# Kernel optimization log

Hardware: AMD Instinct MI355X
Metric: run time of the kernel (lower is better)

The kernel has to match this reference:

```python
import jax, jax.numpy as jnp
import numpy as np

N_NODE = 100_000
N_EDGE = 1_000_000
D = 64          # in_dim = out_dim
A = 64          # attn_dim
B = 8           # batchsize
N_REL = 200     # rel table size = 2*n_rel+1 = 401
N_ENT = 50_000
N_RELTAB = 2 * N_REL + 1


def setup_inputs() -> dict:
    key = jax.random.key(0)
    ks = jax.random.split(key, 16)
    # edges columns: [batch_query_idx, head_ent, rel, tail_ent, sub_local, obj_local]
    r_idx = jax.random.randint(ks[0], (N_EDGE,), 0, B)
    head = jax.random.randint(ks[1], (N_EDGE,), 0, N_ENT)
    rel = jax.random.randint(ks[2], (N_EDGE,), 0, N_RELTAB)
    tail = jax.random.randint(ks[3], (N_EDGE,), 0, N_ENT)
    sub = jax.random.randint(ks[4], (N_EDGE,), 0, N_NODE)
    obj = jax.random.randint(ks[5], (N_EDGE,), 0, N_NODE)
    edges = jnp.stack([r_idx, head, rel, tail, sub, obj], axis=1)
    nodes = jnp.stack([
        jax.random.randint(ks[6], (N_NODE,), 0, B),
        jax.random.randint(ks[7], (N_NODE,), 0, N_ENT)], axis=1)
    s = 1.0 / np.sqrt(D)
    return {
        "q_sub": jax.random.randint(ks[8], (B,), 0, N_ENT),
        "q_rel": jax.random.randint(ks[9], (B,), 0, N_RELTAB),
        "hidden": jax.random.normal(ks[10], (N_NODE, D), jnp.float32),
        "edges": edges,
        "nodes": nodes,
        "old_nodes_new_idx": jax.random.randint(ks[11], (50_000,), 0, N_NODE),
        "batchsize": B,
        "rel_emb": jax.random.normal(ks[12], (N_RELTAB, D), jnp.float32) * s,
        "Ws": jax.random.normal(ks[13], (A, D), jnp.float32) * s,
        "Wr": jax.random.normal(ks[14], (A, D), jnp.float32) * s,
        "Wqr_w": jax.random.normal(ks[15], (A, D), jnp.float32) * s,
        "Wqr_b": jnp.zeros((A,), jnp.float32),
        "walpha_w": jax.random.normal(jax.random.fold_in(key, 101), (1, A), jnp.float32) * (1.0 / np.sqrt(A)),
        "walpha_b": jnp.zeros((1,), jnp.float32),
        "Wh": jax.random.normal(jax.random.fold_in(key, 102), (D, D), jnp.float32) * s,
    }


def reference(q_sub, q_rel, hidden, edges, nodes, old_nodes_new_idx, batchsize,
              rel_emb, Ws, Wr, Wqr_w, Wqr_b, walpha_w, walpha_b, Wh):
    sub = edges[:, 4]   # local source node index [E]
    rel = edges[:, 2]   # relation index        [E]
    obj = edges[:, 5]   # local target node     [E]
    r_idx = edges[:, 0]  # which query each edge belongs to [E]

    hs = hidden[sub]                 # [E, D] gather of node hidden states
    hr = rel_emb[rel]                # [E, D] relation embedding (rela_embed(h, r) = rel_emb[r])
    h_qr = rel_emb[q_rel][r_idx]     # [E, D] query relation embedding per edge

    # attention MLP: sigmoid(w_alpha @ relu(Ws hs + Wr hr + Wqr h_qr + b))
    pre = (jnp.einsum('ed,ad->ea', hs, Ws)
           + jnp.einsum('ed,ad->ea', hr, Wr)
           + jnp.einsum('ed,ad->ea', h_qr, Wqr_w) + Wqr_b)        # [E, A]
    alpha = jax.nn.sigmoid(jnp.einsum('ea,oa->eo', jax.nn.relu(pre), walpha_w) + walpha_b)  # [E, 1]

    message = alpha * (hs + hr)      # [E, D]
    n_node = hidden.shape[0]
    message_agg = jax.ops.segment_sum(message, obj, num_segments=n_node)  # [N, D]
    hidden_new = jnp.einsum('nd,od->no', message_agg, Wh)  # act = identity
    return hidden_new
```

## Files before the change

kernel.cpp:

```cpp
#include <hip/hip_runtime.h>
#include <cstdint>
#include <cstddef>

#define DD 64
#define N_RELTAB 401
#define N_QR 8
#define T_ROWS (N_RELTAB + N_QR)
#define T_U16_STRIDE 66

__device__ __forceinline__ uint16_t f2bf(float f) {
    uint32_t u = __float_as_uint(f);
    u += 0x7fffu + ((u >> 16) & 1u);
    return (uint16_t)(u >> 16);
}
__device__ __forceinline__ float bf2f(uint16_t u) {
    return __uint_as_float(((uint32_t)u) << 16);
}

__global__ __launch_bounds__(64) void build_T(
    const float* __restrict__ rel_emb, const float* __restrict__ Wr,
    const float* __restrict__ Wqr_w, const float* __restrict__ Wqr_b,
    const int* __restrict__ q_rel, uint16_t* __restrict__ T)
{
    int r = blockIdx.x, a = threadIdx.x;
    const float* w;
    const float* src;
    float acc;
    if (r < N_RELTAB) { w = Wr + a * DD; src = rel_emb + r * DD; acc = 0.f; }
    else {
        int k = r - N_RELTAB;
        w = Wqr_w + a * DD;
        src = rel_emb + q_rel[k] * DD;
        acc = Wqr_b[a];
    }
#pragma unroll
    for (int d = 0; d < DD; ++d) acc = fmaf(src[d], w[d], acc);
    T[r * T_U16_STRIDE + a] = f2bf(acc);
}

__global__ __launch_bounds__(256) void rowmat(
    const float* __restrict__ in, const float* __restrict__ W,
    float* __restrict__ out, int nrows)
{
    int n = blockIdx.x * 256 + threadIdx.x;
    if (n >= nrows) return;
    float row[DD];
    const float4* rp = (const float4*)(in + ((size_t)n << 6));
#pragma unroll
    for (int j = 0; j < DD / 4; ++j) {
        float4 v = rp[j];
        row[4*j+0] = v.x; row[4*j+1] = v.y; row[4*j+2] = v.z; row[4*j+3] = v.w;
    }
    float4* op = (float4*)(out + ((size_t)n << 6));
    for (int a0 = 0; a0 < DD; a0 += 4) {
        const float* w0 = W + a0 * DD;
        float s0 = 0.f, s1 = 0.f, s2 = 0.f, s3 = 0.f;
#pragma unroll
        for (int d = 0; d < DD; ++d) {
            float r = row[d];
            s0 = fmaf(w0[d],          r, s0);
            s1 = fmaf(w0[DD + d],     r, s1);
            s2 = fmaf(w0[2 * DD + d], r, s2);
            s3 = fmaf(w0[3 * DD + d], r, s3);
        }
        float4 o; o.x = s0; o.y = s1; o.z = s2; o.w = s3;
        op[a0 >> 2] = o;
    }
}

__global__ __launch_bounds__(256) void hist_kernel(
    const int* __restrict__ edges, int* __restrict__ counts, int n_edge)
{
    int e = blockIdx.x * 256 + threadIdx.x;
    if (e < n_edge) atomicAdd(&counts[edges[6 * e + 5]], 1);
}

__global__ __launch_bounds__(1024) void scan1(
    const int* __restrict__ counts, int* __restrict__ offsets,
    int* __restrict__ bsums, int n)
{
    __shared__ int wsum[16];
    int t = threadIdx.x, i = blockIdx.x * 1024 + t;
    int lane = t & 63, wid = t >> 6;
    int c = (i < n) ? counts[i] : 0;
    int v = c;
#pragma unroll
    for (int d = 1; d < 64; d <<= 1) { int u = __shfl_up(v, d); if (lane >= d) v += u; }
    if (lane == 63) wsum[wid] = v;
    __syncthreads();
    if (wid == 0) {
        int s = (lane < 16) ? wsum[lane] : 0;
#pragma unroll
        for (int d = 1; d < 16; d <<= 1) { int u = __shfl_up(s, d); if (lane >= d) s += u; }
        if (lane < 16) wsum[lane] = s;
    }
    __syncthreads();
    int woff = (wid == 0) ? 0 : wsum[wid - 1];
    if (i < n) offsets[i] = woff + v - c;
    if (t == 1023) bsums[blockIdx.x] = wsum[15];
}

__global__ void scan2(const int* __restrict__ bsums, int* __restrict__ boffs, int nb)
{
    if (threadIdx.x == 0 && blockIdx.x == 0) {
        int s = 0;
        for (int i = 0; i < nb; ++i) { boffs[i] = s; s += bsums[i]; }
    }
}

__global__ __launch_bounds__(1024) void scan3(
    int* __restrict__ offsets, int* __restrict__ cursor,
    const int* __restrict__ boffs, int n)
{
    int i = blockIdx.x * 1024 + threadIdx.x;
    if (i < n) {
        int v = offsets[i] + boffs[blockIdx.x];
        offsets[i] = v;
        cursor[i] = v;
    }
}

__global__ __launch_bounds__(256) void build_sorted(
    const int* __restrict__ edges, int* __restrict__ cursor,
    uint32_t* __restrict__ sorted, int n_edge)
{
    int e = blockIdx.x * 256 + threadIdx.x;
    if (e >= n_edge) return;
    const int2* ep = (const int2*)(edges + 6 * e);
    int ridx = ep[0].x;
    int rel  = ep[1].x;
    int2 so  = ep[2];
    int pos = atomicAdd(&cursor[so.y], 1);
    sorted[pos] = (uint32_t)so.x | ((uint32_t)rel << 17) | ((uint32_t)ridx << 26);
}

__global__ __launch_bounds__(256) void aggregate(
    const uint32_t* __restrict__ sorted, const int* __restrict__ offsets,
    const int* __restrict__ counts, const float* __restrict__ X,
    const float* __restrict__ hidden, const uint16_t* __restrict__ T,
    const float* __restrict__ rel_emb, const float* __restrict__ walpha_w,
    const float* __restrict__ walpha_b, float* __restrict__ agg, int n_node)
{
    __shared__ float sQ[N_QR * DD];
    int tid = threadIdx.x;
    int lane = tid & 63, wid = tid >> 6;
    for (int i = tid; i < N_QR * DD; i += 256)
        sQ[i] = bf2f(T[(N_RELTAB + (i >> 6)) * T_U16_STRIDE + (i & 63)]);
    __syncthreads();

    float wa = walpha_w[lane];
    float wb = walpha_b[0];

    int n = blockIdx.x * 4 + wid;
    if (n >= n_node) return;
    int start = offsets[n];
    int cnt   = counts[n];
    float acc = 0.f;
    for (int i = 0; i < cnt; ++i) {
        uint32_t p = sorted[start + i];
        int sub  = (int)(p & 0x1FFFFu);
        int rel  = (int)((p >> 17) & 0x1FFu);
        int ridx = (int)(p >> 26);
        float x = X[((size_t)sub << 6) + lane];
        float h = hidden[((size_t)sub << 6) + lane];
        float c = bf2f(T[rel * T_U16_STRIDE + lane]);
        float q = sQ[(ridx << 6) + lane];
        float r = rel_emb[(rel << 6) + lane];
        float t = fmaxf(x + c + q, 0.f) * wa;
#pragma unroll
        for (int off = 32; off; off >>= 1) t += __shfl_xor(t, off);
        float alpha = 1.f / (1.f + __expf(-(t + wb)));
        acc = fmaf(alpha, h + r, acc);
    }
    agg[((size_t)n << 6) + lane] = acc;
}

extern "C" void kernel_launch(void* const* d_in, const int* in_sizes, int n_in,
                              void* d_out, int out_size, void* d_ws, size_t ws_size,
                              hipStream_t stream)
{
    const int*   q_rel    = (const int*)d_in[1];
    const float* hidden   = (const float*)d_in[2];
    const int*   edges    = (const int*)d_in[3];
    const float* rel_emb  = (const float*)d_in[7];
    const float* Ws       = (const float*)d_in[8];
    const float* Wr       = (const float*)d_in[9];
    const float* Wqr_w    = (const float*)d_in[10];
    const float* Wqr_b    = (const float*)d_in[11];
    const float* walpha_w = (const float*)d_in[12];
    const float* walpha_b = (const float*)d_in[13];
    const float* Wh       = (const float*)d_in[14];
    float* out = (float*)d_out;

    const int n_node = in_sizes[2] / DD;
    const int n_edge = in_sizes[3] / 6;
    const int NB = (n_node + 1023) / 1024;

    char* w = (char*)d_ws;
    float*    X       = (float*)w;               w += (size_t)n_node * DD * 4;
    float*    agg     = (float*)w;               w += (size_t)n_node * DD * 4;
    uint32_t* sorted  = (uint32_t*)w;            w += (size_t)n_edge * 4;
    int*      counts  = (int*)w;                 w += (size_t)n_node * 4;
    int*      offsets = (int*)w;                 w += (size_t)n_node * 4;
    int*      cursor  = (int*)w;                 w += (size_t)n_node * 4;
    int*      bsums   = (int*)w;                 w += 4096;
    int*      boffs   = (int*)w;                 w += 4096;
    uint16_t* T       = (uint16_t*)w;

    build_T<<<T_ROWS, 64, 0, stream>>>(rel_emb, Wr, Wqr_w, Wqr_b, q_rel, T);
    rowmat<<<(n_node + 255) / 256, 256, 0, stream>>>(hidden, Ws, X, n_node);
    hipMemsetAsync(counts, 0, (size_t)n_node * 4, stream);
    hist_kernel<<<(n_edge + 255) / 256, 256, 0, stream>>>(edges, counts, n_edge);
    scan1<<<NB, 1024, 0, stream>>>(counts, offsets, bsums, n_node);
    scan2<<<1, 64, 0, stream>>>(bsums, boffs, NB);
    scan3<<<NB, 1024, 0, stream>>>(offsets, cursor, boffs, n_node);
    build_sorted<<<(n_edge + 255) / 256, 256, 0, stream>>>(edges, cursor, sorted, n_edge);
    aggregate<<<(n_node + 3) / 4, 256, 0, stream>>>(sorted, offsets, counts, X, hidden,
                                                    T, rel_emb, walpha_w, walpha_b,
                                                    agg, n_node);
    rowmat<<<(n_node + 255) / 256, 256, 0, stream>>>(agg, Wh, out, n_node);
}
```

Measured before the change: 455.4 us.

## Switch aggregation to edge-chunked waves with per-edge alpha and segmented writes

Replaces the one-wave-per-node aggregation with fixed 64-edge chunks per wave. Each chunk computes its attention pre-activations into shared memory as fp16 and reduces them per lane, which removes the per-edge shuffle reductions. It then does a segmented accumulation over the obj-sorted edges, using atomics only at chunk-boundary segments. This balances work across waves regardless of node degree. In exchange it adds a full memset of agg, doubles the sorted key size to carry obj, stores C in fp32 instead of bf16, and replaces the serial block-offset scan with a parallel one.

Measured after the change: 460.5 us. About the same (+1.1%).

```diff
diff --git a/kernel.cpp b/kernel.cpp
--- a/kernel.cpp
+++ b/kernel.cpp
@@ -1,4 +1,5 @@
 #include <hip/hip_runtime.h>
+#include <hip/hip_fp16.h>
 #include <cstdint>
 #include <cstddef>
 
@@ -6,26 +7,15 @@
 #define N_RELTAB 401
 #define N_QR 8
 #define T_ROWS (N_RELTAB + N_QR)
-#define T_U16_STRIDE 66
-
-__device__ __forceinline__ uint16_t f2bf(float f) {
-    uint32_t u = __float_as_uint(f);
-    u += 0x7fffu + ((u >> 16) & 1u);
-    return (uint16_t)(u >> 16);
-}
-__device__ __forceinline__ float bf2f(uint16_t u) {
-    return __uint_as_float(((uint32_t)u) << 16);
-}
-
-__global__ __launch_bounds__(64) void build_T(
+#define WPB 4
+
+__global__ __launch_bounds__(64) void build_C(
     const float* __restrict__ rel_emb, const float* __restrict__ Wr,
     const float* __restrict__ Wqr_w, const float* __restrict__ Wqr_b,
-    const int* __restrict__ q_rel, uint16_t* __restrict__ T)
+    const int* __restrict__ q_rel, float* __restrict__ Cf)
 {
     int r = blockIdx.x, a = threadIdx.x;
-    const float* w;
-    const float* src;
-    float acc;
+    const float* w; const float* src; float acc;
     if (r < N_RELTAB) { w = Wr + a * DD; src = rel_emb + r * DD; acc = 0.f; }
     else {
         int k = r - N_RELTAB;
@@ -35,7 +25,7 @@
     }
 #pragma unroll
     for (int d = 0; d < DD; ++d) acc = fmaf(src[d], w[d], acc);
-    T[r * T_U16_STRIDE + a] = f2bf(acc);
+    Cf[r * DD + a] = acc;
 }
 
 __global__ __launch_bounds__(256) void rowmat(
@@ -100,12 +90,26 @@
     if (t == 1023) bsums[blockIdx.x] = wsum[15];
 }
 
-__global__ void scan2(const int* __restrict__ bsums, int* __restrict__ boffs, int nb)
-{
-    if (threadIdx.x == 0 && blockIdx.x == 0) {
-        int s = 0;
-        for (int i = 0; i < nb; ++i) { boffs[i] = s; s += bsums[i]; }
-    }
+__global__ __launch_bounds__(1024) void scan_small(
+    const int* __restrict__ bsums, int* __restrict__ boffs, int nb)
+{
+    __shared__ int wsum[16];
+    int t = threadIdx.x, lane = t & 63, wid = t >> 6;
+    int c = (t < nb) ? bsums[t] : 0;
+    int v = c;
+#pragma unroll
+    for (int d = 1; d < 64; d <<= 1) { int u = __shfl_up(v, d); if (lane >= d) v += u; }
+    if (lane == 63) wsum[wid] = v;
+    __syncthreads();
+    if (wid == 0) {
+        int s = (lane < 16) ? wsum[lane] : 0;
+#pragma unroll
+        for (int d = 1; d < 16; d <<= 1) { int u = __shfl_up(s, d); if (lane >= d) s += u; }
+        if (lane < 16) wsum[lane] = s;
+    }
+    __syncthreads();
+    int woff = (wid == 0) ? 0 : wsum[wid - 1];
+    if (t < nb) boffs[t] = woff + v - c;
 }
 
 __global__ __launch_bounds__(1024) void scan3(
@@ -122,7 +126,7 @@
 
 __global__ __launch_bounds__(256) void build_sorted(
     const int* __restrict__ edges, int* __restrict__ cursor,
-    uint32_t* __restrict__ sorted, int n_edge)
+    uint64_t* __restrict__ sorted, int n_edge)
 {
     int e = blockIdx.x * 256 + threadIdx.x;
     if (e >= n_edge) return;
@@ -131,48 +135,81 @@
     int rel  = ep[1].x;
     int2 so  = ep[2];
     int pos = atomicAdd(&cursor[so.y], 1);
-    sorted[pos] = (uint32_t)so.x | ((uint32_t)rel << 17) | ((uint32_t)ridx << 26);
-}
-
-__global__ __launch_bounds__(256) void aggregate(
-    const uint32_t* __restrict__ sorted, const int* __restrict__ offsets,
-    const int* __restrict__ counts, const float* __restrict__ X,
-    const float* __restrict__ hidden, const uint16_t* __restrict__ T,
+    uint32_t pay = (uint32_t)so.x | ((uint32_t)rel << 17) | ((uint32_t)ridx << 26);
+    sorted[pos] = (uint64_t)pay | ((uint64_t)(uint32_t)so.y << 32);
+}
+
+__global__ __launch_bounds__(64 * WPB) void fused_aggregate(
+    const uint64_t* __restrict__ sorted, const float* __restrict__ X,
+    const float* __restrict__ hidden, const float* __restrict__ Cf,
     const float* __restrict__ rel_emb, const float* __restrict__ walpha_w,
-    const float* __restrict__ walpha_b, float* __restrict__ agg, int n_node)
+    const float* __restrict__ walpha_b, float* __restrict__ agg,
+    int n_edge, int n_node)
 {
     __shared__ float sQ[N_QR * DD];
+    __shared__ uint2 hdr[WPB][DD];
+    __shared__ __half sS[WPB][DD][DD + 2];
     int tid = threadIdx.x;
     int lane = tid & 63, wid = tid >> 6;
-    for (int i = tid; i < N_QR * DD; i += 256)
-        sQ[i] = bf2f(T[(N_RELTAB + (i >> 6)) * T_U16_STRIDE + (i & 63)]);
+    for (int i = tid; i < N_QR * DD; i += 64 * WPB) sQ[i] = Cf[N_RELTAB * DD + i];
+
+    long wchunk = (long)blockIdx.x * WPB + wid;
+    long e = wchunk * DD + lane;
+    uint64_t p = (e < n_edge) ? sorted[e]
+                              : ((uint64_t)(uint32_t)n_node << 32);
+    hdr[wid][lane] = make_uint2((uint32_t)p, (uint32_t)(p >> 32));
     __syncthreads();
 
     float wa = walpha_w[lane];
     float wb = walpha_b[0];
 
-    int n = blockIdx.x * 4 + wid;
-    if (n >= n_node) return;
-    int start = offsets[n];
-    int cnt   = counts[n];
+#pragma unroll 4
+    for (int j = 0; j < DD; ++j) {
+        uint32_t pj = __builtin_amdgcn_readfirstlane(hdr[wid][j].x);
+        int sub  = (int)(pj & 0x1FFFFu);
+        int rel  = (int)((pj >> 17) & 0x1FFu);
+        int ridx = (int)((pj >> 26) & 7u);
+        float x = X[((size_t)sub << 6) + lane];
+        float c = Cf[(rel << 6) + lane];
+        float q = sQ[(ridx << 6) + lane];
+        sS[wid][j][lane] = __float2half(fmaxf(x + c + q, 0.f) * wa);
+    }
+    __syncthreads();
+
+    float t = 0.f;
+    const __half2* row2 = (const __half2*)&sS[wid][lane][0];
+#pragma unroll
+    for (int a2 = 0; a2 < DD / 2; ++a2) {
+        float2 f = __half22float2(row2[a2]);
+        t += f.x + f.y;
+    }
+    float alpha_l = 1.f / (1.f + __expf(-(t + wb)));
+
     float acc = 0.f;
-    for (int i = 0; i < cnt; ++i) {
-        uint32_t p = sorted[start + i];
-        int sub  = (int)(p & 0x1FFFFu);
-        int rel  = (int)((p >> 17) & 0x1FFu);
-        int ridx = (int)(p >> 26);
-        float x = X[((size_t)sub << 6) + lane];
-        float h = hidden[((size_t)sub << 6) + lane];
-        float c = bf2f(T[rel * T_U16_STRIDE + lane]);
-        float q = sQ[(ridx << 6) + lane];
-        float r = rel_emb[(rel << 6) + lane];
-        float t = fmaxf(x + c + q, 0.f) * wa;
-#pragma unroll
-        for (int off = 32; off; off >>= 1) t += __shfl_xor(t, off);
-        float alpha = 1.f / (1.f + __expf(-(t + wb)));
-        acc = fmaf(alpha, h + r, acc);
-    }
-    agg[((size_t)n << 6) + lane] = acc;
+    int prev = (int)__builtin_amdgcn_readfirstlane(hdr[wid][0].y);
+    bool firstseg = true;
+    for (int j = 0; j < DD; ++j) {
+        uint32_t pj = __builtin_amdgcn_readfirstlane(hdr[wid][j].x);
+        int oj      = (int)__builtin_amdgcn_readfirstlane(hdr[wid][j].y);
+        if (oj != prev) {
+            if (prev < n_node) {
+                if (firstseg) atomicAdd(&agg[((size_t)prev << 6) + lane], acc);
+                else          agg[((size_t)prev << 6) + lane] = acc;
+            }
+            firstseg = false;
+            acc = 0.f;
+            prev = oj;
+        }
+        if (oj < n_node) {
+            int sub = (int)(pj & 0x1FFFFu);
+            int rel = (int)((pj >> 17) & 0x1FFu);
+            float h = hidden[((size_t)sub << 6) + lane];
+            float r = rel_emb[(rel << 6) + lane];
+            float aj = __uint_as_float(__builtin_amdgcn_readlane(__float_as_uint(alpha_l), j));
+            acc = fmaf(aj, h + r, acc);
+        }
+    }
+    if (prev < n_node) atomicAdd(&agg[((size_t)prev << 6) + lane], acc);
 }
 
 extern "C" void kernel_launch(void* const* d_in, const int* in_sizes, int n_in,
@@ -197,26 +234,27 @@
     const int NB = (n_node + 1023) / 1024;
 
     char* w = (char*)d_ws;
-    float*    X       = (float*)w;               w += (size_t)n_node * DD * 4;
-    float*    agg     = (float*)w;               w += (size_t)n_node * DD * 4;
-    uint32_t* sorted  = (uint32_t*)w;            w += (size_t)n_edge * 4;
-    int*      counts  = (int*)w;                 w += (size_t)n_node * 4;
-    int*      offsets = (int*)w;                 w += (size_t)n_node * 4;
-    int*      cursor  = (int*)w;                 w += (size_t)n_node * 4;
-    int*      bsums   = (int*)w;                 w += 4096;
-    int*      boffs   = (int*)w;                 w += 4096;
-    uint16_t* T       = (uint16_t*)w;
-
-    build_T<<<T_ROWS, 64, 0, stream>>>(rel_emb, Wr, Wqr_w, Wqr_b, q_rel, T);
+    float*    X       = (float*)w;     w += (size_t)n_node * DD * 4;
+    float*    agg     = (float*)w;     w += (size_t)n_node * DD * 4;
+    uint64_t* sorted  = (uint64_t*)w;  w += (size_t)n_edge * 8;
+    int*      counts  = (int*)w;       w += (size_t)n_node * 4;
+    int*      offsets = (int*)w;       w += (size_t)n_node * 4;
+    int*      cursor  = (int*)w;       w += (size_t)n_node * 4;
+    int*      bsums   = (int*)w;       w += 4096;
+    int*      boffs   = (int*)w;       w += 4096;
+    float*    Cf      = (float*)w;     w += (size_t)T_ROWS * DD * 4;
+
+    build_C<<<T_ROWS, 64, 0, stream>>>(rel_emb, Wr, Wqr_w, Wqr_b, q_rel, Cf);
     rowmat<<<(n_node + 255) / 256, 256, 0, stream>>>(hidden, Ws, X, n_node);
     hipMemsetAsync(counts, 0, (size_t)n_node * 4, stream);
+    hipMemsetAsync(agg, 0, (size_t)n_node * DD * 4, stream);
     hist_kernel<<<(n_edge + 255) / 256, 256, 0, stream>>>(edges, counts, n_edge);
     scan1<<<NB, 1024, 0, stream>>>(counts, offsets, bsums, n_node);
-    scan2<<<1, 64, 0, stream>>>(bsums, boffs, NB);
+    scan_small<<<1, 1024, 0, stream>>>(bsums, boffs, NB);
     scan3<<<NB, 1024, 0, stream>>>(offsets, cursor, boffs, n_node);
     build_sorted<<<(n_edge + 255) / 256, 256, 0, stream>>>(edges, cursor, sorted, n_edge);
-    aggregate<<<(n_node + 3) / 4, 256, 0, stream>>>(sorted, offsets, counts, X, hidden,
-                                                    T, rel_emb, walpha_w, walpha_b,
-                                                    agg, n_node);
+    const int nwaves = (n_edge + DD - 1) / DD;
+    fused_aggregate<<<(nwaves + WPB - 1) / WPB, 64 * WPB, 0, stream>>>(
+        sorted, X, hidden, Cf, rel_emb, walpha_w, walpha_b, agg, n_edge, n_node);
     rowmat<<<(n_node + 255) / 256, 256, 0, stream>>>(agg, Wh, out, n_node);
 }
```
